# Kernel optimization log

Measured on AMD Instinct MI355X. Metric: run time of the kernel, lower is better.

## Reference

```python
import math
import jax, jax.numpy as jnp
import numpy as np

B, N, D = 16, 2048, 256
EPS = 1e-8  # torch cosine_similarity default eps
TAU = 3.0   # gumbel-softmax temperature


def setup_inputs() -> dict:
    key = jax.random.key(0)
    k1, k2 = jax.random.split(key)
    return {
        "LowLevelFeatures": jax.random.normal(k1, (B, 1, N, D), dtype=jnp.float32),
        "HighLevelFeatures": jax.random.normal(k2, (B, 1, N, D), dtype=jnp.float32),
        "batch_size": B,
    }


def _forward(LLF4, HLF4):
    LLF = LLF4[:, 0]  # [B,N,D]
    HLF = HLF4[:, 0]  # [B,N,D]
    b, n, d = LLF.shape
    # pairwise cosine similarity [B,N,N]: matmul + norm-product (same math as
    # torch's broadcast cosine_similarity, without the [B,N,N,D] intermediate)
    dots = jnp.einsum('bnd,bmd->bnm', LLF, HLF)
    nl = jnp.linalg.norm(LLF, axis=-1)  # [B,N]
    nh = jnp.linalg.norm(HLF, axis=-1)  # [B,N]
    sim = dots / jnp.maximum(nl[:, :, None] * nh[:, None, :], EPS)
    sim = sim / math.sqrt(d)
    probs = jax.nn.softmax(sim, axis=1)  # softmax over dim 1 (LLF rows)
    # F.gumbel_softmax(probs, tau=3, hard=True, dim=1): probs act as logits
    u = jax.random.uniform(jax.random.key(42), probs.shape,
                           minval=1e-10, maxval=1.0)
    gumbels = -jnp.log(-jnp.log(u))
    y_soft = jax.nn.softmax((probs + gumbels) / TAU, axis=1)
    idx = jnp.argmax(y_soft, axis=1)  # [B,N]: selected LLF-row n per HLF col m
    # torch.where on the one-hot scans row-major over (b, n, m), so per batch
    # the returned n-indices are the SORTED multiset of selected indices
    sl = jnp.sort(idx, axis=-1)  # [B,N]
    bidx = jnp.arange(b)[:, None]  # [B,1]
    aligned = HLF[bidx, sl]  # gather along dim 1 -> [B,N,D]
    # rowwise cosine similarity between gathered HLF and LLF
    w = jnp.sum(aligned * LLF, axis=-1) / jnp.maximum(
        jnp.linalg.norm(aligned, axis=-1) * nl, EPS)  # [B,N]
    noise = jax.nn.softmax(w / 0.1, axis=1)[:, :, None]  # [B,N,1]
    hlf_new = aligned + LLF * noise
    out = HLF.at[bidx, sl].set(hlf_new)
    return out


def reference(LowLevelFeatures, HighLevelFeatures, batch_size):
    return _forward(LowLevelFeatures, HighLevelFeatures)
```

## Files before the change

### kernel.cpp

```cpp
#include <hip/hip_runtime.h>
#include <math.h>

#define NB 16
#define NN 2048
#define ND 256
#define BNtot (NB*NN)
#define HH 33554432u

typedef __attribute__((ext_vector_type(8))) short bf16x8;
typedef __attribute__((ext_vector_type(4))) float f32x4;

__device__ __forceinline__ void gld16(const void* g, void* l){
  __builtin_amdgcn_global_load_lds((const __attribute__((address_space(1))) void*)g,
                                   (__attribute__((address_space(3))) void*)l, 16, 0, 0);
}

__device__ __forceinline__ unsigned rotl(unsigned v, int r){
  return __builtin_amdgcn_alignbit(v, v, 32-r);
}
__device__ __forceinline__ unsigned umaxu(unsigned a, unsigned b){ return a > b ? a : b; }
__device__ __forceinline__ unsigned uminu(unsigned a, unsigned b){ return a < b ? a : b; }

__device__ __forceinline__ float gumbelv(unsigned b, unsigned n, unsigned m){
  unsigned f = (b<<22) | (n<<11) | m;
  unsigned x0 = (b < 8u) ? f : (f - HH);
  unsigned x1 = x0 + HH;
  const unsigned ks0=0u, ks1=42u, ks2=0u^42u^0x1BD11BDAu;
  unsigned v0 = x0 + ks0;
  unsigned v1 = x1 + ks1;
#define TFR(r) { v0 += v1; v1 = rotl(v1,(r)); v1 ^= v0; }
  TFR(13) TFR(15) TFR(26) TFR(6)
  v0 += ks1; v1 += ks2 + 1u;
  TFR(17) TFR(29) TFR(16) TFR(24)
  v0 += ks2; v1 += ks0 + 2u;
  TFR(13) TFR(15) TFR(26) TFR(6)
  v0 += ks0; v1 += ks1 + 3u;
  TFR(17) TFR(29) TFR(16) TFR(24)
  v0 += ks1; v1 += ks2 + 4u;
  TFR(13) TFR(15) TFR(26) TFR(6)
  v0 += ks2; v1 += ks0 + 5u;
#undef TFR
  unsigned bits = (b < 8u) ? v0 : v1;
  float fl = __uint_as_float((bits>>9) | 0x3F800000u) - 1.0f;
  float u = fmaxf(1e-10f, fl + 1e-10f);
  return -logf(-logf(u));
}

__device__ __forceinline__ float gfromkey(unsigned key){
  float fl = __uint_as_float(key | 0x3F800000u) - 1.0f;
  float u = fmaxf(1e-10f, fl + 1e-10f);
  return -logf(-logf(u));
}

__device__ __forceinline__ void gumbel_body(int gb, float* __restrict__ pcv, int* __restrict__ pci){
  int t    = gb*256 + (int)threadIdx.x;
  int half = t & 1;
  int m    = (t >> 1) & 2047;
  int bl   = (t >> 12) & 7;
  int nq   = t >> 15;
  int chunkbase = nq << 7;
  int nstart = chunkbase + (half << 6);
  unsigned x0 = ((unsigned)bl << 22) | ((unsigned)nstart << 11) | (unsigned)m;
  const unsigned KS2 = 42u ^ 0x1BD11BDAu;
  unsigned a1=0, a2=0, c1=0, c2=0;
  unsigned vk = (unsigned)(127 - (half<<6));
#define TFR(r)       { v0 += v1; v1 = rotl(v1,(r)); v1 ^= v0; }
#define TFRI(r, inj) { v0 += v1 + (inj); v1 = rotl(v1,(r)); v1 ^= v0; }
  #pragma unroll 4
  for (int j = 0; j < 64; ++j){
    unsigned v0 = x0;
    unsigned v1 = x0 + (HH + 42u);
    TFR(13) TFR(15) TFR(26) TFR(6)
    v1 += KS2 + 1u;
    TFRI(17, 42u) TFR(29) TFR(16) TFR(24)
    v1 += 2u;
    TFRI(13, KS2) TFR(15) TFR(26) TFR(6)
    v1 += 42u + 3u;
    TFR(17) TFR(29) TFR(16) TFR(24)
    v1 += KS2 + 4u;
    TFRI(13, 42u) TFR(15) TFR(26) TFR(6)
    v0 += KS2; v1 += 5u;
    unsigned pa = (v0 & 0xFFFFFE00u) | (vk & 0x1FFu);
    unsigned pb = (v1 & 0xFFFFFE00u) | (vk & 0x1FFu);
    unsigned ta = uminu(pa, a1);
    a1 = umaxu(pa, a1);
    a2 = umaxu(ta, a2);
    unsigned tc = uminu(pb, c1);
    c1 = umaxu(pb, c1);
    c2 = umaxu(tc, c2);
    x0 += 2048u;
    vk -= 1u;
  }
#undef TFR
#undef TFRI
  unsigned p1 = __shfl_xor((int)a1, 1), p2 = __shfl_xor((int)a2, 1);
  unsigned q1 = __shfl_xor((int)c1, 1), q2 = __shfl_xor((int)c2, 1);
  unsigned A1 = umaxu(a1, p1);
  unsigned A2 = umaxu(uminu(a1, p1), umaxu(a2, p2));
  unsigned C1 = umaxu(c1, q1);
  unsigned C2 = umaxu(uminu(c1, q1), umaxu(c2, q2));
  if (half == 0){
    int baseA = (((nq*NB + bl  )*NN + m) << 1);
    int baseB = (((nq*NB + bl+8)*NN + m) << 1);
    pcv[baseA+0] = gfromkey(A1 >> 9); pci[baseA+0] = chunkbase + 127 - (int)(A1 & 127u);
    pcv[baseA+1] = gfromkey(A2 >> 9); pci[baseA+1] = chunkbase + 127 - (int)(A2 & 127u);
    pcv[baseB+0] = gfromkey(C1 >> 9); pci[baseB+0] = chunkbase + 127 - (int)(C1 & 127u);
    pcv[baseB+1] = gfromkey(C2 >> 9); pci[baseB+1] = chunkbase + 127 - (int)(C2 & 127u);
  }
}

__launch_bounds__(256)
__global__ void kgumbel(float* __restrict__ pcv, int* __restrict__ pci){
  gumbel_body(blockIdx.x, pcv, pci);
}

__global__ void knorms(const float* __restrict__ LLF, const float* __restrict__ HLF,
                       float* __restrict__ nl, float* __restrict__ nh){
  int row = blockIdx.x;
  int wave = threadIdx.x >> 6;
  int lane = threadIdx.x & 63;
  const float* src = wave ? HLF : LLF;
  float4 v = ((const float4*)(src + (size_t)row*ND))[lane];
  float s = v.x*v.x + v.y*v.y + v.z*v.z + v.w*v.w;
  for (int o=32;o;o>>=1) s += __shfl_down(s,o);
  if (lane==0) (wave? nh: nl)[row] = sqrtf(s);
}

__launch_bounds__(256)
__global__ void kfuse1(const float* __restrict__ LLF, const float* __restrict__ HLF,
                       ushort* __restrict__ Abf, ushort* __restrict__ Bbf,
                       float* __restrict__ nl, float* __restrict__ nh,
                       float* __restrict__ pcv, int* __restrict__ pci){
  int bid = blockIdx.x;
  int g = bid / 9, r = bid - g*9;
  if (r == 0){ gumbel_body(g, pcv, pci); return; }
  int pid = g*8 + (r-1);
  int px  = pid & 8191;
  int py  = pid >> 13;
  int w    = threadIdx.x >> 6;
  int lane = threadIdx.x & 63;
  int row = px*4 + w;
  const float* src = py ? HLF : LLF;
  ushort* dst      = py ? Bbf : Abf;
  float4 v = ((const float4*)(src + (size_t)row*ND))[lane];
  float s = v.x*v.x + v.y*v.y + v.z*v.z + v.w*v.w;
  for (int o=32;o;o>>=1) s += __shfl_down(s,o);
  if (lane==0) (py ? nh : nl)[row] = sqrtf(s);
  uint2 u;
  u.x = (__float_as_uint(v.y)&0xFFFF0000u)|(__float_as_uint(v.x)>>16);
  u.y = (__float_as_uint(v.w)&0xFFFF0000u)|(__float_as_uint(v.z)>>16);
  int b = row >> 11, nloc = row & 2047;
  int k = lane << 2;
  int ck = k >> 6;
  int j  = k & 63;
  int qi = j >> 3;
  size_t off = (size_t)b*524288 + (size_t)ck*131072 + (size_t)nloc*64
             + ((qi ^ (nloc & 7)) << 3) + (j & 7);
  *(uint2*)(dst + off) = u;
}

#define K1 0.09016844f
__launch_bounds__(256)
__global__ void kgemm_dma(const ushort* __restrict__ Abf, const ushort* __restrict__ Bbf,
                          const float* __restrict__ nl, const float* __restrict__ nh,
                          float* __restrict__ partS){
  __shared__ ushort As[128*64];
  __shared__ ushort Bs[128*64];
  __shared__ float colsum[128];
  const int b  = blockIdx.z;
  const int n0 = blockIdx.y << 7;
  const int m0 = blockIdx.x << 7;
  const int tid  = threadIdx.x;
  const int lane = tid & 63;
  const int w    = tid >> 6;
  const int wn   = w >> 1, wm = w & 1;
  const int quad = lane >> 4, l15 = lane & 15;
  if (tid < 128) colsum[tid] = 0.0f;

  const ushort* Ab = Abf + (size_t)b*524288;
  const ushort* Bb = Bbf + (size_t)b*524288;

  f32x4 acc[4][4];
  #pragma unroll
  for (int i=0;i<4;i++)
    #pragma unroll
    for (int j=0;j<4;j++) acc[i][j] = (f32x4){0.f,0.f,0.f,0.f};

  for (int ck=0; ck<4; ck++){
    __syncthreads();
    const ushort* ga = Ab + (size_t)ck*131072 + (size_t)n0*64;
    const ushort* gb = Bb + (size_t)ck*131072 + (size_t)m0*64;
    #pragma unroll
    for (int t=0;t<4;t++){
      int seg = (w*4 + t) * 512;
      gld16(ga + seg + lane*8, &As[seg]);
      gld16(gb + seg + lane*8, &Bs[seg]);
    }
    __syncthreads();
    #pragma unroll
    for (int ks=0; ks<64; ks+=32){
      bf16x8 af[4], bf[4];
      #pragma unroll
      for (int t=0;t<4;t++){
        int R = wn*64 + t*16 + l15;
        af[t] = *(const bf16x8*)(&As[R*64 + ((((ks>>3)+quad) ^ (R&7))<<3)]);
      }
      #pragma unroll
      for (int t=0;t<4;t++){
        int R = wm*64 + t*16 + l15;
        bf[t] = *(const bf16x8*)(&Bs[R*64 + ((((ks>>3)+quad) ^ (R&7))<<3)]);
      }
      #pragma unroll
      for (int ti=0;ti<4;ti++)
        #pragma unroll
        for (int tj=0;tj<4;tj++)
          acc[ti][tj] = __builtin_amdgcn_mfma_f32_16x16x32_bf16(af[ti], bf[tj], acc[ti][tj], 0, 0, 0);
    }
  }

  float an[4][4];
  #pragma unroll
  for (int ti=0;ti<4;ti++)
    #pragma unroll
    for (int r=0;r<4;r++)
      an[ti][r] = K1 / nl[b*NN + n0 + wn*64 + ti*16 + quad*4 + r];
  float bm[4];
  #pragma unroll
  for (int tj=0;tj<4;tj++)
    bm[tj] = 1.0f / nh[b*NN + m0 + wm*64 + tj*16 + l15];
  #pragma unroll
  for (int tj=0;tj<4;tj++){
    float s = 0.0f;
    #pragma unroll
    for (int ti=0;ti<4;ti++)
      #pragma unroll
      for (int r=0;r<4;r++)
        s += __builtin_amdgcn_exp2f(acc[ti][tj][r]*an[ti][r]*bm[tj] - K1);
    s += __shfl_down(s, 32);
    s += __shfl_down(s, 16);
    if (lane < 16) atomicAdd(&colsum[wm*64 + tj*16 + l15], s);
  }
  __syncthreads();
  if (tid < 128)
    partS[(size_t)blockIdx.y*BNtot + b*NN + m0 + tid] = colsum[tid];
}

__launch_bounds__(256)
__global__ void kgemm_mfma(const float* __restrict__ LLF, const float* __restrict__ HLF,
                           const float* __restrict__ nl, const float* __restrict__ nh,
                           float* __restrict__ partS){
  __shared__ ushort As[128][72];
  __shared__ ushort Bs[128][72];
  __shared__ float colsum[128];
  const int b  = blockIdx.z;
  const int n0 = blockIdx.y << 7;
  const int m0 = blockIdx.x << 7;
  const float* Ab = LLF + (size_t)b*NN*ND;
  const float* Bb = HLF + (size_t)b*NN*ND;
  const int tid  = threadIdx.x;
  const int lane = tid & 63;
  const int w    = tid >> 6;
  const int wn   = w >> 1, wm = w & 1;
  const int quad = lane >> 4, l15 = lane & 15;
  if (tid < 128) colsum[tid] = 0.0f;

  f32x4 acc[4][4];
  #pragma unroll
  for (int i=0;i<4;i++)
    #pragma unroll
    for (int j=0;j<4;j++) acc[i][j] = (f32x4){0.f,0.f,0.f,0.f};

  const int rbase = tid >> 3;
  const int kq    = (tid & 7) << 3;

  for (int ck=0; ck<4; ck++){
    const int k0 = ck << 6;
    __syncthreads();
    #pragma unroll
    for (int pi=0; pi<4; pi++){
      int row = rbase + (pi<<5);
      const float* pa = Ab + (size_t)(n0+row)*ND + k0 + kq;
      float4 a0 = *(const float4*)pa;
      float4 a1 = *(const float4*)(pa+4);
      uint4 ua;
      ua.x = (__float_as_uint(a0.y)&0xFFFF0000u)|(__float_as_uint(a0.x)>>16);
      ua.y = (__float_as_uint(a0.w)&0xFFFF0000u)|(__float_as_uint(a0.z)>>16);
      ua.z = (__float_as_uint(a1.y)&0xFFFF0000u)|(__float_as_uint(a1.x)>>16);
      ua.w = (__float_as_uint(a1.w)&0xFFFF0000u)|(__float_as_uint(a1.z)>>16);
      *(uint4*)(&As[row][kq]) = ua;
      const float* pb = Bb + (size_t)(m0+row)*ND + k0 + kq;
      float4 b0 = *(const float4*)pb;
      float4 b1 = *(const float4*)(pb+4);
      uint4 ub;
      ub.x = (__float_as_uint(b0.y)&0xFFFF0000u)|(__float_as_uint(b0.x)>>16);
      ub.y = (__float_as_uint(b0.w)&0xFFFF0000u)|(__float_as_uint(b0.z)>>16);
      ub.z = (__float_as_uint(b1.y)&0xFFFF0000u)|(__float_as_uint(b1.x)>>16);
      ub.w = (__float_as_uint(b1.w)&0xFFFF0000u)|(__float_as_uint(b1.z)>>16);
      *(uint4*)(&Bs[row][kq]) = ub;
    }
    __syncthreads();
    #pragma unroll
    for (int ks=0; ks<64; ks+=32){
      bf16x8 af[4], bf[4];
      #pragma unroll
      for (int t=0;t<4;t++)
        af[t] = *(const bf16x8*)(&As[wn*64 + t*16 + l15][ks + quad*8]);
      #pragma unroll
      for (int t=0;t<4;t++)
        bf[t] = *(const bf16x8*)(&Bs[wm*64 + t*16 + l15][ks + quad*8]);
      #pragma unroll
      for (int ti=0;ti<4;ti++)
        #pragma unroll
        for (int tj=0;tj<4;tj++)
          acc[ti][tj] = __builtin_amdgcn_mfma_f32_16x16x32_bf16(af[ti], bf[tj], acc[ti][tj], 0, 0, 0);
    }
  }

  float an[4][4];
  #pragma unroll
  for (int ti=0;ti<4;ti++)
    #pragma unroll
    for (int r=0;r<4;r++)
      an[ti][r] = K1 / nl[b*NN + n0 + wn*64 + ti*16 + quad*4 + r];
  float bm[4];
  #pragma unroll
  for (int tj=0;tj<4;tj++)
    bm[tj] = 1.0f / nh[b*NN + m0 + wm*64 + tj*16 + l15];
  #pragma unroll
  for (int tj=0;tj<4;tj++){
    float s = 0.0f;
    #pragma unroll
    for (int ti=0;ti<4;ti++)
      #pragma unroll
      for (int r=0;r<4;r++)
        s += __builtin_amdgcn_exp2f(acc[ti][tj][r]*an[ti][r]*bm[tj] - K1);
    s += __shfl_down(s, 32);
    s += __shfl_down(s, 16);
    if (lane < 16) atomicAdd(&colsum[wm*64 + tj*16 + l15], s);
  }
  __syncthreads();
  if (tid < 128)
    partS[(size_t)blockIdx.y*BNtot + b*NN + m0 + tid] = colsum[tid];
}

__launch_bounds__(256)
__global__ void kresolve(const float* __restrict__ LLF, const float* __restrict__ HLF,
                         const float* __restrict__ nl, const float* __restrict__ nh,
                         const float* __restrict__ partS,
                         const float* __restrict__ pcv, const int* __restrict__ pci,
                         int* __restrict__ idx){
  int w    = threadIdx.x >> 6;
  int lane = threadIdx.x & 63;
  int g = blockIdx.x*4 + w;
  int b = g >> 11, m = g & 2047;
  float ps = (lane < 16) ? partS[(size_t)lane*BNtot + g] : 0.0f;
  ps += __shfl_down(ps, 8);
  ps += __shfl_down(ps, 4);
  ps += __shfl_down(ps, 2);
  ps += __shfl_down(ps, 1);
  float invS = 1.0f / __shfl(ps, 0);
  float pv = -INFINITY; int pn = 0;
  if (lane < 32){
    int base = ((((lane>>1)*NB + b)*NN + m) << 1) + (lane & 1);
    pv = pcv[base]; pn = pci[base];
  }
  float gmax = pv;
  for (int o=32;o;o>>=1) gmax = fmaxf(gmax, __shfl_down(gmax,o));
  gmax = __shfl(gmax, 0);
  unsigned long long mask = __ballot(pv >= gmax - 8e-5f);
  mask &= 0xFFFFFFFFull;
  float4 h = ((const float4*)(HLF + (size_t)g*ND))[lane];
  float nhg = nh[g];
  float bestQ = -INFINITY; int bestN = 1<<30;
  while (mask){
    int src = __builtin_ctzll(mask); mask &= mask-1;
    int   n  = __shfl(pn, src);
    float gv = __shfl(pv, src);
    float4 a = ((const float4*)(LLF + ((size_t)b*NN + n)*ND))[lane];
    float d = a.x*h.x + a.y*h.y + a.z*h.z + a.w*h.w;
    for (int o=32;o;o>>=1) d += __shfl_down(d,o);
    d = __shfl(d, 0);
    float sim = (d / fmaxf(nl[b*NN+n]*nhg, 1e-8f)) * 0.0625f;
    float q = expf(sim - 0.0625f)*invS + gv;
    if (q > bestQ || (q == bestQ && n < bestN)){ bestQ = q; bestN = n; }
  }
  if (lane==0) idx[g] = bestN;
}

__launch_bounds__(256)
__global__ void kstats(const float* __restrict__ A, const float* __restrict__ Bm,
                       const float* __restrict__ nl, const float* __restrict__ nh,
                       float* __restrict__ Mout, float* __restrict__ Sinv){
  __shared__ float As[64][33];
  __shared__ float Bs[64][33];
  __shared__ float Cs[64][65];
  const int b  = blockIdx.x >> 5;
  const int m0 = (blockIdx.x & 31) << 6;
  const float* Ab = A  + (size_t)b*NN*ND;
  const float* Bb = Bm + (size_t)b*NN*ND;
  const int tid = threadIdx.x;
  const int tx = tid & 15, ty = tid >> 4;
  float nhv[4];
  #pragma unroll
  for (int j=0;j<4;j++) nhv[j] = nh[b*NN + m0 + tx*4 + j];
  float Mr = -INFINITY, Sr = 0.0f;
  for (int nt=0; nt<NN; nt+=64){
    float acc[4][4] = {{0.f,0.f,0.f,0.f},{0.f,0.f,0.f,0.f},{0.f,0.f,0.f,0.f},{0.f,0.f,0.f,0.f}};
    for (int kc=0; kc<ND; kc+=32){
      __syncthreads();
      #pragma unroll
      for (int s=0;s<2;s++){
        int f = tid + (s<<8);
        int r = f >> 3;
        int c = (f & 7) << 2;
        float4 va = *(const float4*)(Ab + (size_t)(nt+r)*ND + kc + c);
        As[r][c]=va.x; As[r][c+1]=va.y; As[r][c+2]=va.z; As[r][c+3]=va.w;
        float4 vb = *(const float4*)(Bb + (size_t)(m0+r)*ND + kc + c);
        Bs[r][c]=vb.x; Bs[r][c+1]=vb.y; Bs[r][c+2]=vb.z; Bs[r][c+3]=vb.w;
      }
      __syncthreads();
      #pragma unroll 4
      for (int k=0;k<32;k++){
        float a0=As[ty*4+0][k], a1=As[ty*4+1][k], a2=As[ty*4+2][k], a3=As[ty*4+3][k];
        float b0=Bs[tx*4+0][k], b1=Bs[tx*4+1][k], b2=Bs[tx*4+2][k], b3=Bs[tx*4+3][k];
        acc[0][0]+=a0*b0; acc[0][1]+=a0*b1; acc[0][2]+=a0*b2; acc[0][3]+=a0*b3;
        acc[1][0]+=a1*b0; acc[1][1]+=a1*b1; acc[1][2]+=a1*b2; acc[1][3]+=a1*b3;
        acc[2][0]+=a2*b0; acc[2][1]+=a2*b1; acc[2][2]+=a2*b2; acc[2][3]+=a2*b3;
        acc[3][0]+=a3*b0; acc[3][1]+=a3*b1; acc[3][2]+=a3*b2; acc[3][3]+=a3*b3;
      }
    }
    float nlv[4];
    #pragma unroll
    for (int i=0;i<4;i++) nlv[i] = nl[b*NN + nt + ty*4 + i];
    __syncthreads();
    #pragma unroll
    for (int i=0;i<4;i++)
      #pragma unroll
      for (int j=0;j<4;j++){
        float denom = fmaxf(nlv[i]*nhv[j], 1e-8f);
        Cs[ty*4+i][tx*4+j] = (acc[i][j]/denom)*0.0625f;
      }
    __syncthreads();
    if (tid < 64){
      float tmax = -INFINITY;
      #pragma unroll 8
      for (int r=0;r<64;r++) tmax = fmaxf(tmax, Cs[r][tid]);
      float newM = fmaxf(Mr, tmax);
      float s = 0.0f;
      #pragma unroll 4
      for (int r=0;r<64;r++) s += expf(Cs[r][tid]-newM);
      Sr = Sr*expf(Mr-newM) + s;
      Mr = newM;
    }
  }
  if (tid < 64){
    Mout[b*NN+m0+tid] = Mr;
    Sinv[b*NN+m0+tid] = 1.0f/Sr;
  }
}

__launch_bounds__(256)
__global__ void kargmax(const float* __restrict__ A, const float* __restrict__ Bm,
                        const float* __restrict__ nl, const float* __restrict__ nh,
                        const float* __restrict__ Mv, const float* __restrict__ Sv,
                        int* __restrict__ idxout){
  __shared__ float As[64][33];
  __shared__ float Bs[64][33];
  __shared__ float Vs[16][64];
  __shared__ int   Is[16][64];
  const int b  = blockIdx.x >> 5;
  const int m0 = (blockIdx.x & 31) << 6;
  const float* Ab = A  + (size_t)b*NN*ND;
  const float* Bb = Bm + (size_t)b*NN*ND;
  const int tid = threadIdx.x;
  const int tx = tid & 15, ty = tid >> 4;
  float nhv[4], Mj[4], iSj[4];
  #pragma unroll
  for (int j=0;j<4;j++){
    int m = m0 + tx*4 + j;
    nhv[j] = nh[b*NN + m];
    Mj[j]  = Mv[b*NN + m];
    iSj[j] = Sv[b*NN + m];
  }
  float bestV = -INFINITY; int bestN = 0;
  for (int nt=0; nt<NN; nt+=64){
    float acc[4][4] = {{0.f,0.f,0.f,0.f},{0.f,0.f,0.f,0.f},{0.f,0.f,0.f,0.f},{0.f,0.f,0.f,0.f}};
    for (int kc=0; kc<ND; kc+=32){
      __syncthreads();
      #pragma unroll
      for (int s=0;s<2;s++){
        int f = tid + (s<<8);
        int r = f >> 3;
        int c = (f & 7) << 2;
        float4 va = *(const float4*)(Ab + (size_t)(nt+r)*ND + kc + c);
        As[r][c]=va.x; As[r][c+1]=va.y; As[r][c+2]=va.z; As[r][c+3]=va.w;
        float4 vb = *(const float4*)(Bb + (size_t)(m0+r)*ND + kc + c);
        Bs[r][c]=vb.x; Bs[r][c+1]=vb.y; Bs[r][c+2]=vb.z; Bs[r][c+3]=vb.w;
      }
      __syncthreads();
      #pragma unroll 4
      for (int k=0;k<32;k++){
        float a0=As[ty*4+0][k], a1=As[ty*4+1][k], a2=As[ty*4+2][k], a3=As[ty*4+3][k];
        float b0=Bs[tx*4+0][k], b1=Bs[tx*4+1][k], b2=Bs[tx*4+2][k], b3=Bs[tx*4+3][k];
        acc[0][0]+=a0*b0; acc[0][1]+=a0*b1; acc[0][2]+=a0*b2; acc[0][3]+=a0*b3;
        acc[1][0]+=a1*b0; acc[1][1]+=a1*b1; acc[1][2]+=a1*b2; acc[1][3]+=a1*b3;
        acc[2][0]+=a2*b0; acc[2][1]+=a2*b1; acc[2][2]+=a2*b2; acc[2][3]+=a2*b3;
        acc[3][0]+=a3*b0; acc[3][1]+=a3*b1; acc[3][2]+=a3*b2; acc[3][3]+=a3*b3;
      }
    }
    float nlv[4];
    #pragma unroll
    for (int i=0;i<4;i++) nlv[i] = nl[b*NN + nt + ty*4 + i];
    float lv[4]; int li[4];
    #pragma unroll
    for (int j=0;j<4;j++){ lv[j] = -INFINITY; li[j] = 0; }
    #pragma unroll
    for (int i=0;i<4;i++){
      int n = nt + ty*4 + i;
      #pragma unroll
      for (int j=0;j<4;j++){
        float denom = fmaxf(nlv[i]*nhv[j], 1e-8f);
        float sim = (acc[i][j]/denom)*0.0625f;
        float p = expf(sim - Mj[j]) * iSj[j];
        float v = p + gumbelv((unsigned)b, (unsigned)n, (unsigned)(m0 + tx*4 + j));
        if (v > lv[j]) { lv[j] = v; li[j] = n; }
      }
    }
    __syncthreads();
    #pragma unroll
    for (int j=0;j<4;j++){ Vs[ty][tx*4+j]=lv[j]; Is[ty][tx*4+j]=li[j]; }
    __syncthreads();
    if (tid < 64){
      #pragma unroll 4
      for (int t=0;t<16;t++){
        float v = Vs[t][tid];
        if (v > bestV){ bestV = v; bestN = Is[t][tid]; }
      }
    }
  }
  if (tid < 64) idxout[b*NN + m0 + tid] = bestN;
}

__global__ void ksort(const int* __restrict__ idx, int* __restrict__ cntg,
                      int* __restrict__ offg, int* __restrict__ sl){
  __shared__ int c[NN];
  __shared__ int part[256];
  int b = blockIdx.x, tid = threadIdx.x;
  for (int v=tid; v<NN; v+=256) c[v]=0;
  __syncthreads();
  for (int j=tid; j<NN; j+=256) atomicAdd(&c[idx[b*NN+j]], 1);
  __syncthreads();
  int base = tid*8, s=0, lc[8];
  #pragma unroll
  for (int k=0;k<8;k++){ lc[k]=c[base+k]; s+=lc[k]; }
  part[tid]=s; __syncthreads();
  for (int o=1;o<256;o<<=1){
    int v = (tid>=o)? part[tid-o] : 0;
    __syncthreads();
    part[tid]+=v;
    __syncthreads();
  }
  int run = part[tid]-s;
  #pragma unroll
  for (int k=0;k<8;k++){
    int v = base+k;
    cntg[b*NN+v]=lc[k];
    offg[b*NN+v]=run;
    for (int j=0;j<lc[k];j++) sl[b*NN+run+j]=v;
    run += lc[k];
  }
}

__global__ void kw(const float* __restrict__ LLF, const float* __restrict__ HLF,
                   const float* __restrict__ nl, const float* __restrict__ nh,
                   const int* __restrict__ sl, float* __restrict__ w){
  int g = blockIdx.x*4 + (threadIdx.x>>6);
  int lane = threadIdx.x & 63;
  int b = g >> 11;
  int s = sl[g];
  float4 a = ((const float4*)(HLF + ((size_t)b*NN + s)*ND))[lane];
  float4 l = ((const float4*)(LLF + (size_t)g*ND))[lane];
  float d = a.x*l.x + a.y*l.y + a.z*l.z + a.w*l.w;
  for (int o=32;o;o>>=1) d += __shfl_down(d,o);
  if (lane==0){
    float denom = fmaxf(nh[b*NN+s]*nl[g], 1e-8f);
    w[g] = d/denom;
  }
}

__global__ void knoise(const float* __restrict__ w, float* __restrict__ nz){
  int b = blockIdx.x, tid = threadIdx.x;
  __shared__ float sred[4];
  float x[8]; float mx = -INFINITY;
  #pragma unroll
  for (int k=0;k<8;k++){ x[k] = w[b*NN + tid*8 + k] / 0.1f; mx = fmaxf(mx, x[k]); }
  for (int o=32;o;o>>=1) mx = fmaxf(mx, __shfl_down(mx,o));
  mx = __shfl(mx, 0);
  if ((tid&63)==0) sred[tid>>6] = mx;
  __syncthreads();
  mx = fmaxf(fmaxf(sred[0],sred[1]), fmaxf(sred[2],sred[3]));
  __syncthreads();
  float e[8]; float s = 0.f;
  #pragma unroll
  for (int k=0;k<8;k++){ e[k] = expf(x[k]-mx); s += e[k]; }
  for (int o=32;o;o>>=1) s += __shfl_down(s,o);
  s = __shfl(s, 0);
  if ((tid&63)==0) sred[tid>>6] = s;
  __syncthreads();
  s = sred[0]+sred[1]+sred[2]+sred[3];
  #pragma unroll
  for (int k=0;k<8;k++) nz[b*NN + tid*8 + k] = e[k]/s;
}

__global__ void kfinal(const float* __restrict__ LLF, const float* __restrict__ HLF,
                       const int* __restrict__ cnt, const int* __restrict__ off,
                       const float* __restrict__ nz, float* __restrict__ out){
  int row = blockIdx.x;
  int lane = threadIdx.x;
  int b = row >> 11;
  float4 h = ((const float4*)(HLF + (size_t)row*ND))[lane];
  int c = cnt[row];
  if (c > 0){
    int i = off[row] + c - 1;
    float ns = nz[b*NN + i];
    float4 l = ((const float4*)(LLF + ((size_t)(b*NN + i))*ND))[lane];
    h.x += l.x*ns; h.y += l.y*ns; h.z += l.z*ns; h.w += l.w*ns;
  }
  ((float4*)(out + (size_t)row*ND))[lane] = h;
}

extern "C" void kernel_launch(void* const* d_in, const int* in_sizes, int n_in,
                              void* d_out, int out_size, void* d_ws, size_t ws_size,
                              hipStream_t stream){
  const float* LLF = (const float*)d_in[0];
  const float* HLF = (const float*)d_in[1];
  float* out = (float*)d_out;
  float* ws = (float*)d_ws;

  float* nl  = ws;
  float* nh  = ws + 1*(size_t)BNtot;
  float* iS  = ws + 2*(size_t)BNtot;
  int*   idx = (int*)(ws + 3*(size_t)BNtot);
  int*   cnt = (int*)(ws + 4*(size_t)BNtot);
  int*   off = (int*)(ws + 5*(size_t)BNtot);
  int*   sl  = (int*)(ws + 6*(size_t)BNtot);
  float* wv  = ws + 7*(size_t)BNtot;
  float* nz  = ws + 8*(size_t)BNtot;
  float* partS = ws + 9*(size_t)BNtot;
  float* pcv   = partS + 16*(size_t)BNtot;
  int*   pci   = (int*)(pcv + 32*(size_t)BNtot);
  ushort* Abf  = (ushort*)(pci + 32*(size_t)BNtot);
  ushort* Bbf  = Abf + (size_t)BNtot*ND;
  const size_t needBytes1 = (9 + 16 + 32 + 32) * (size_t)BNtot * 4;
  const size_t needBytes2 = needBytes1 + 2 * (size_t)BNtot * ND * 2;

  if (ws_size >= needBytes2){
    hipLaunchKernelGGL(kfuse1,  dim3(18432),     dim3(256), 0, stream, LLF, HLF, Abf, Bbf, nl, nh, pcv, pci);
    hipLaunchKernelGGL(kgemm_dma,dim3(16,16,16), dim3(256), 0, stream, Abf, Bbf, nl, nh, partS);
    hipLaunchKernelGGL(kresolve,dim3(BNtot/4),   dim3(256), 0, stream, LLF, HLF, nl, nh, partS, pcv, pci, idx);
  } else if (ws_size >= needBytes1){
    hipLaunchKernelGGL(knorms,   dim3(BNtot),      dim3(128), 0, stream, LLF, HLF, nl, nh);
    hipLaunchKernelGGL(kgemm_mfma,dim3(16,16,16),  dim3(256), 0, stream, LLF, HLF, nl, nh, partS);
    hipLaunchKernelGGL(kgumbel,  dim3(2048),       dim3(256), 0, stream, pcv, pci);
    hipLaunchKernelGGL(kresolve, dim3(BNtot/4),    dim3(256), 0, stream, LLF, HLF, nl, nh, partS, pcv, pci, idx);
  } else {
    float* Mv = ws + 9*(size_t)BNtot;
    hipLaunchKernelGGL(knorms,   dim3(BNtot),      dim3(128), 0, stream, LLF, HLF, nl, nh);
    hipLaunchKernelGGL(kstats,   dim3(NB*32),      dim3(256), 0, stream, LLF, HLF, nl, nh, Mv, iS);
    hipLaunchKernelGGL(kargmax,  dim3(NB*32),      dim3(256), 0, stream, LLF, HLF, nl, nh, Mv, iS, idx);
  }

  hipLaunchKernelGGL(ksort,  dim3(NB),      dim3(256), 0, stream, idx, cnt, off, sl);
  hipLaunchKernelGGL(kw,     dim3(BNtot/4), dim3(256), 0, stream, LLF, HLF, nl, nh, sl, wv);
  hipLaunchKernelGGL(knoise, dim3(NB),      dim3(256), 0, stream, wv, nz);
  hipLaunchKernelGGL(kfinal, dim3(BNtot),   dim3(64),  0, stream, LLF, HLF, cnt, off, nz, out);
}
```

Before: 312.9 us.

## Interleave gumbel hashing with row norm/bf16 prep inside each thread

Before, the fused prologue kernel split its blocks into gumbel blocks and row-conversion blocks, 18432 blocks in all. Now each of 2048 blocks does its gumbel work in two halves. Between the halves, each thread loads and converts four LLF rows and then four HLF rows, so the ALU-heavy Philox rounds can overlap with memory latency. The gumbel state is moved into a struct so the loop can be split. It adds an occupancy hint and drops a redundant mask on vk. The risk is fewer blocks and higher register pressure from the eight float4 values kept live per thread.

```diff
diff --git a/kernel.cpp b/kernel.cpp
--- a/kernel.cpp
+++ b/kernel.cpp
@@ -52,22 +52,30 @@
   return -logf(-logf(u));
 }
 
-__device__ __forceinline__ void gumbel_body(int gb, float* __restrict__ pcv, int* __restrict__ pci){
-  int t    = gb*256 + (int)threadIdx.x;
-  int half = t & 1;
-  int m    = (t >> 1) & 2047;
-  int bl   = (t >> 12) & 7;
-  int nq   = t >> 15;
-  int chunkbase = nq << 7;
-  int nstart = chunkbase + (half << 6);
-  unsigned x0 = ((unsigned)bl << 22) | ((unsigned)nstart << 11) | (unsigned)m;
+struct GumState {
+  unsigned x0, vk, a1, a2, c1, c2;
+  int t;
+};
+
+__device__ __forceinline__ void gum_init(GumState& g, int gb){
+  g.t = gb*256 + (int)threadIdx.x;
+  int half = g.t & 1;
+  int m    = (g.t >> 1) & 2047;
+  int bl   = (g.t >> 12) & 7;
+  int nq   = g.t >> 15;
+  int nstart = (nq << 7) + (half << 6);
+  g.x0 = ((unsigned)bl << 22) | ((unsigned)nstart << 11) | (unsigned)m;
+  g.a1 = g.a2 = g.c1 = g.c2 = 0;
+  g.vk = (unsigned)(127 - (half<<6));
+}
+
+__device__ __forceinline__ void gum_iter(GumState& g, const int cnt){
   const unsigned KS2 = 42u ^ 0x1BD11BDAu;
-  unsigned a1=0, a2=0, c1=0, c2=0;
-  unsigned vk = (unsigned)(127 - (half<<6));
+  unsigned x0=g.x0, vk=g.vk, a1=g.a1, a2=g.a2, c1=g.c1, c2=g.c2;
 #define TFR(r)       { v0 += v1; v1 = rotl(v1,(r)); v1 ^= v0; }
 #define TFRI(r, inj) { v0 += v1 + (inj); v1 = rotl(v1,(r)); v1 ^= v0; }
   #pragma unroll 4
-  for (int j = 0; j < 64; ++j){
+  for (int j = 0; j < cnt; ++j){
     unsigned v0 = x0;
     unsigned v1 = x0 + (HH + 42u);
     TFR(13) TFR(15) TFR(26) TFR(6)
@@ -80,8 +88,8 @@
     v1 += KS2 + 4u;
     TFRI(13, 42u) TFR(15) TFR(26) TFR(6)
     v0 += KS2; v1 += 5u;
-    unsigned pa = (v0 & 0xFFFFFE00u) | (vk & 0x1FFu);
-    unsigned pb = (v1 & 0xFFFFFE00u) | (vk & 0x1FFu);
+    unsigned pa = (v0 & 0xFFFFFE00u) | vk;
+    unsigned pb = (v1 & 0xFFFFFE00u) | vk;
     unsigned ta = uminu(pa, a1);
     a1 = umaxu(pa, a1);
     a2 = umaxu(ta, a2);
@@ -93,12 +101,22 @@
   }
 #undef TFR
 #undef TFRI
-  unsigned p1 = __shfl_xor((int)a1, 1), p2 = __shfl_xor((int)a2, 1);
-  unsigned q1 = __shfl_xor((int)c1, 1), q2 = __shfl_xor((int)c2, 1);
-  unsigned A1 = umaxu(a1, p1);
-  unsigned A2 = umaxu(uminu(a1, p1), umaxu(a2, p2));
-  unsigned C1 = umaxu(c1, q1);
-  unsigned C2 = umaxu(uminu(c1, q1), umaxu(c2, q2));
+  g.x0=x0; g.vk=vk; g.a1=a1; g.a2=a2; g.c1=c1; g.c2=c2;
+}
+
+__device__ __forceinline__ void gum_finish(const GumState& g, float* __restrict__ pcv,
+                                           int* __restrict__ pci){
+  int half = g.t & 1;
+  int m    = (g.t >> 1) & 2047;
+  int bl   = (g.t >> 12) & 7;
+  int nq   = g.t >> 15;
+  int chunkbase = nq << 7;
+  unsigned p1 = __shfl_xor((int)g.a1, 1), p2 = __shfl_xor((int)g.a2, 1);
+  unsigned q1 = __shfl_xor((int)g.c1, 1), q2 = __shfl_xor((int)g.c2, 1);
+  unsigned A1 = umaxu(g.a1, p1);
+  unsigned A2 = umaxu(uminu(g.a1, p1), umaxu(g.a2, p2));
+  unsigned C1 = umaxu(g.c1, q1);
+  unsigned C2 = umaxu(uminu(g.c1, q1), umaxu(g.c2, q2));
   if (half == 0){
     int baseA = (((nq*NB + bl  )*NN + m) << 1);
     int baseB = (((nq*NB + bl+8)*NN + m) << 1);
@@ -111,7 +129,31 @@
 
 __launch_bounds__(256)
 __global__ void kgumbel(float* __restrict__ pcv, int* __restrict__ pci){
-  gumbel_body(blockIdx.x, pcv, pci);
+  GumState g; gum_init(g, blockIdx.x);
+  gum_iter(g, 64);
+  gum_finish(g, pcv, pci);
+}
+
+__device__ __forceinline__ void prep_rows(const float4* v, int wid, int lane,
+                                          ushort* __restrict__ dst, float* __restrict__ nrm){
+  #pragma unroll
+  for (int i=0;i<4;i++){
+    int row = wid*4 + i;
+    float s = v[i].x*v[i].x + v[i].y*v[i].y + v[i].z*v[i].z + v[i].w*v[i].w;
+    for (int o=32;o;o>>=1) s += __shfl_down(s,o);
+    if (lane==0) nrm[row] = sqrtf(s);
+    uint2 u;
+    u.x = (__float_as_uint(v[i].y)&0xFFFF0000u)|(__float_as_uint(v[i].x)>>16);
+    u.y = (__float_as_uint(v[i].w)&0xFFFF0000u)|(__float_as_uint(v[i].z)>>16);
+    int b = row >> 11, nloc = row & 2047;
+    int k = lane << 2;
+    int ck = k >> 6;
+    int j  = k & 63;
+    int qi = j >> 3;
+    size_t off = (size_t)b*524288 + (size_t)ck*131072 + (size_t)nloc*64
+               + ((qi ^ (nloc & 7)) << 3) + (j & 7);
+    *(uint2*)(dst + off) = u;
+  }
 }
 
 __global__ void knorms(const float* __restrict__ LLF, const float* __restrict__ HLF,
@@ -126,37 +168,28 @@
   if (lane==0) (wave? nh: nl)[row] = sqrtf(s);
 }
 
-__launch_bounds__(256)
+__launch_bounds__(256, 8)
 __global__ void kfuse1(const float* __restrict__ LLF, const float* __restrict__ HLF,
                        ushort* __restrict__ Abf, ushort* __restrict__ Bbf,
                        float* __restrict__ nl, float* __restrict__ nh,
                        float* __restrict__ pcv, int* __restrict__ pci){
-  int bid = blockIdx.x;
-  int g = bid / 9, r = bid - g*9;
-  if (r == 0){ gumbel_body(g, pcv, pci); return; }
-  int pid = g*8 + (r-1);
-  int px  = pid & 8191;
-  int py  = pid >> 13;
-  int w    = threadIdx.x >> 6;
-  int lane = threadIdx.x & 63;
-  int row = px*4 + w;
-  const float* src = py ? HLF : LLF;
-  ushort* dst      = py ? Bbf : Abf;
-  float4 v = ((const float4*)(src + (size_t)row*ND))[lane];
-  float s = v.x*v.x + v.y*v.y + v.z*v.z + v.w*v.w;
-  for (int o=32;o;o>>=1) s += __shfl_down(s,o);
-  if (lane==0) (py ? nh : nl)[row] = sqrtf(s);
-  uint2 u;
-  u.x = (__float_as_uint(v.y)&0xFFFF0000u)|(__float_as_uint(v.x)>>16);
-  u.y = (__float_as_uint(v.w)&0xFFFF0000u)|(__float_as_uint(v.z)>>16);
-  int b = row >> 11, nloc = row & 2047;
-  int k = lane << 2;
-  int ck = k >> 6;
-  int j  = k & 63;
-  int qi = j >> 3;
-  size_t off = (size_t)b*524288 + (size_t)ck*131072 + (size_t)nloc*64
-             + ((qi ^ (nloc & 7)) << 3) + (j & 7);
-  *(uint2*)(dst + off) = u;
+  int t = blockIdx.x*256 + (int)threadIdx.x;
+  int wid = t >> 6;
+  int lane = t & 63;
+  GumState g; gum_init(g, blockIdx.x);
+  float4 va[4];
+  #pragma unroll
+  for (int i=0;i<4;i++)
+    va[i] = ((const float4*)(LLF + (size_t)(wid*4+i)*ND))[lane];
+  gum_iter(g, 32);
+  prep_rows(va, wid, lane, Abf, nl);
+  float4 vb[4];
+  #pragma unroll
+  for (int i=0;i<4;i++)
+    vb[i] = ((const float4*)(HLF + (size_t)(wid*4+i)*ND))[lane];
+  gum_iter(g, 32);
+  prep_rows(vb, wid, lane, Bbf, nh);
+  gum_finish(g, pcv, pci);
 }
 
 #define K1 0.09016844f
@@ -655,7 +688,7 @@
   const size_t needBytes2 = needBytes1 + 2 * (size_t)BNtot * ND * 2;
 
   if (ws_size >= needBytes2){
-    hipLaunchKernelGGL(kfuse1,  dim3(18432),     dim3(256), 0, stream, LLF, HLF, Abf, Bbf, nl, nh, pcv, pci);
+    hipLaunchKernelGGL(kfuse1,  dim3(2048),      dim3(256), 0, stream, LLF, HLF, Abf, Bbf, nl, nh, pcv, pci);
     hipLaunchKernelGGL(kgemm_dma,dim3(16,16,16), dim3(256), 0, stream, Abf, Bbf, nl, nh, partS);
     hipLaunchKernelGGL(kresolve,dim3(BNtot/4),   dim3(256), 0, stream, LLF, HLF, nl, nh, partS, pcv, pci, idx);
   } else if (ws_size >= needBytes1){
```

After: 284.0 us. -9.2%, faster.
